# Performance work log

Hardware: AMD Instinct MI355X
Metric: run time of the kernel (lower is better)

Reference implementation:

```python
import jax, jax.numpy as jnp
import numpy as np
from jax import lax

EPS = 1e-5
BETA = 0.25  # commitment cost

def _conv(x, w, b):
    y = lax.conv_general_dilated(x, w, (1, 1), 'VALID',
                                 dimension_numbers=('NCHW', 'OIHW', 'NCHW'))
    return y + b[None, :, None, None]

def _maxpool2(x):
    return lax.reduce_window(x, -jnp.inf, lax.max, (1, 1, 2, 2), (1, 1, 2, 2), 'VALID')

def _bn(x, scale, bias):
    # training-mode batch norm over (N, H, W)
    mean = jnp.mean(x, axis=(0, 2, 3), keepdims=True)
    var = jnp.var(x, axis=(0, 2, 3), keepdims=True)
    xhat = (x - mean) * lax.rsqrt(var + EPS)
    return xhat * scale[None, :, None, None] + bias[None, :, None, None]

def _vq(z_nchw, codebook):
    # z: [B,32,4,4] -> vectors [B*16, 32]
    B, C, H, W = z_nchw.shape
    z = jnp.transpose(z_nchw, (0, 2, 3, 1)).reshape(-1, C)          # [N, D]
    # squared L2 distances to codebook [K, D]
    d = (jnp.sum(z * z, axis=1, keepdims=True)
         + jnp.sum(codebook * codebook, axis=1)
         - 2.0 * z @ codebook.T)                                    # [N, K]
    idx = jnp.argmin(d, axis=1)                                     # [N]
    q = codebook[idx]                                               # [N, D]
    sg = lax.stop_gradient
    vq_loss = jnp.mean((q - sg(z)) ** 2) + BETA * jnp.mean((sg(q) - z) ** 2)
    q_st = z + sg(q - z)                                            # straight-through
    recon = jnp.transpose(q_st.reshape(B, H, W, C), (0, 3, 1, 2))
    return recon, vq_loss

def setup_inputs() -> dict:
    key = jax.random.key(0)
    ks = jax.random.split(key, 12)
    f = lambda k, shape, s: (jax.random.normal(k, shape, jnp.float32) * s)
    inp = {
        'x': jax.random.normal(ks[0], (2048, 3, 32, 32), jnp.float32),
        'conv1_w': f(ks[1], (64, 3, 3, 3), 0.1), 'conv1_b': jnp.zeros((64,), jnp.float32),
        'bn1_scale': jnp.ones((64,), jnp.float32), 'bn1_bias': jnp.zeros((64,), jnp.float32),
        'conv2_w': f(ks[2], (32, 64, 3, 3), 0.05), 'conv2_b': jnp.zeros((32,), jnp.float32),
        'bn2_scale': jnp.ones((32,), jnp.float32), 'bn2_bias': jnp.zeros((32,), jnp.float32),
        'conv3_w': f(ks[3], (32, 32, 3, 3), 0.06), 'conv3_b': jnp.zeros((32,), jnp.float32),
        'bn3_scale': jnp.ones((32,), jnp.float32), 'bn3_bias': jnp.zeros((32,), jnp.float32),
        'codebook': f(ks[4], (100, 32), 0.5),
        'fc1_w': f(ks[5], (64, 512), 0.04), 'fc1_b': jnp.zeros((64,), jnp.float32),
        'fc2_w': f(ks[6], (10, 64), 0.12), 'fc2_b': jnp.zeros((10,), jnp.float32),
    }
    return inp

def reference(x, conv1_w, conv1_b, bn1_scale, bn1_bias,
              conv2_w, conv2_b, bn2_scale, bn2_bias,
              conv3_w, conv3_b, bn3_scale, bn3_bias,
              codebook, fc1_w, fc1_b, fc2_w, fc2_b):
    h = _bn(jax.nn.relu(_maxpool2(_conv(x, conv1_w, conv1_b))), bn1_scale, bn1_bias)
    h = _bn(jax.nn.relu(_maxpool2(_conv(h, conv2_w, conv2_b))), bn2_scale, bn2_bias)
    h = _bn(jax.nn.relu(_conv(h, conv3_w, conv3_b)), bn3_scale, bn3_bias)   # [B,32,4,4]
    recon, vq_loss = _vq(h, codebook)
    blended = 0.5 * recon + h
    flat = blended.reshape(-1, 4 * 4 * 32)
    z1 = jax.nn.relu(flat @ fc1_w.T + fc1_b)
    y = z1 @ fc2_w.T + fc2_b
    return recon, h, vq_loss, jax.nn.log_softmax(y, axis=1)
```

## Files before the change

kernel.cpp:

```cpp
#include <hip/hip_runtime.h>
#include <math.h>


#define CNT1 460800.0
#define CNT2 73728.0
#define CNT3 32768.0

__global__ void k0_w2t(const float* __restrict__ w2, float* __restrict__ w2t)
{
  const int idx = blockIdx.x * 256 + threadIdx.x;
  const int half = idx & 1, cog = (idx >> 1) & 15;
  const int r = (idx >> 5) % 72, cc = idx / 2304;
  const int o = cog + 16 * half;
  w2t[idx] = w2[o * 576 + cc * 72 + r];
}

template<int CB, int W4, int J0, int CNT>
__device__ __forceinline__ void conv1_seg(const float* img, const float* wr,
                                          int prow, float bias, float* vout)
{
  float acc[CNT][4];
#pragma unroll
  for (int j = 0; j < CNT; ++j) { acc[j][0] = 0; acc[j][1] = 0; acc[j][2] = 0; acc[j][3] = 0; }
#pragma unroll
  for (int cin = 0; cin < 3; ++cin) {
    float pt[4][4 * W4];
    const float4* src = (const float4*)&img[cin * 1024 + (2 * prow) * 32 + CB];
#pragma unroll
    for (int r = 0; r < 4; ++r)
#pragma unroll
      for (int u = 0; u < W4; ++u) {
        float4 f = src[r * 8 + u];
        pt[r][u * 4 + 0] = f.x; pt[r][u * 4 + 1] = f.y;
        pt[r][u * 4 + 2] = f.z; pt[r][u * 4 + 3] = f.w;
      }
#pragma unroll
    for (int jj = 0; jj < CNT; ++jj) {
      const int c0 = 2 * (J0 + jj) - CB;
#pragma unroll
      for (int kh = 0; kh < 3; ++kh)
#pragma unroll
        for (int kw = 0; kw < 3; ++kw) {
          const float w_ = wr[cin * 9 + kh * 3 + kw];
          acc[jj][0] += pt[kh][c0 + kw] * w_;
          acc[jj][1] += pt[kh][c0 + 1 + kw] * w_;
          acc[jj][2] += pt[kh + 1][c0 + kw] * w_;
          acc[jj][3] += pt[kh + 1][c0 + 1 + kw] * w_;
        }
    }
  }
#pragma unroll
  for (int jj = 0; jj < CNT; ++jj) {
    float v = fmaxf(fmaxf(acc[jj][0], acc[jj][1]), fmaxf(acc[jj][2], acc[jj][3])) + bias;
    vout[J0 + jj] = fmaxf(v, 0.f);
  }
}

__global__ __launch_bounds__(256) void k1_conv1(
    const float* __restrict__ x, const float* __restrict__ w1,
    const float* __restrict__ b1, double* __restrict__ dstats,
    float* __restrict__ y1)
{
  __shared__ float img[3072];
  __shared__ float red_s[256], red_q[256];
  const int n = blockIdx.x, t = threadIdx.x;
  const float4* xin = (const float4*)(x + n * 3072);
  float4* img4 = (float4*)img;
  for (int i = t; i < 768; i += 256) img4[i] = xin[i];
  const int ch = t & 63, rslot = t >> 6;
  float wr[27];
#pragma unroll
  for (int k = 0; k < 27; ++k) wr[k] = w1[ch * 27 + k];
  const float bias = b1[ch];
  __syncthreads();
  float s = 0.f, ss = 0.f;
  for (int prow = rslot; prow < 15; prow += 4) {
    float vout[15];
    conv1_seg<0, 4, 0, 7>(img, wr, prow, bias, vout);
    conv1_seg<12, 4, 7, 5>(img, wr, prow, bias, vout);
    conv1_seg<24, 2, 12, 3>(img, wr, prow, bias, vout);
    float4* dst = (float4*)(y1 + n * 15360 + ch * 240 + prow * 16);
    dst[0] = make_float4(vout[0], vout[1], vout[2], vout[3]);
    dst[1] = make_float4(vout[4], vout[5], vout[6], vout[7]);
    dst[2] = make_float4(vout[8], vout[9], vout[10], vout[11]);
    dst[3] = make_float4(vout[12], vout[13], vout[14], 0.f);
#pragma unroll
    for (int j = 0; j < 15; ++j) { s += vout[j]; ss += vout[j] * vout[j]; }
  }
  red_s[t] = s; red_q[t] = ss;
  __syncthreads();
  if (t < 64) {
    float rs = red_s[t] + red_s[t + 64] + red_s[t + 128] + red_s[t + 192];
    float rq = red_q[t] + red_q[t + 64] + red_q[t + 128] + red_q[t + 192];
    atomicAdd(&dstats[t * 16], (double)rs);
    atomicAdd(&dstats[t * 16 + 8], (double)rq);
  }
}

__global__ __launch_bounds__(256) void k1_conv1_stats(
    const float* __restrict__ x, const float* __restrict__ w1,
    const float* __restrict__ b1, double* __restrict__ dstats)
{
  __shared__ float img[3072];
  __shared__ float red[512];
  const int n = blockIdx.x, t = threadIdx.x;
  const float4* xin = (const float4*)(x + n * 3072);
  float4* img4 = (float4*)img;
  for (int i = t; i < 768; i += 256) img4[i] = xin[i];
  const int c = t >> 2, q = t & 3;
  float wr[27];
#pragma unroll
  for (int k = 0; k < 27; ++k) wr[k] = w1[c * 27 + k];
  const float bias = b1[c];
  __syncthreads();
  float s = 0.f, ss = 0.f;
  for (int p = q; p < 225; p += 4) {
    const int i = p / 15, j = p % 15;
    float a0 = 0, a1 = 0, a2 = 0, a3 = 0;
#pragma unroll
    for (int cin = 0; cin < 3; ++cin) {
      float pt[4][4];
#pragma unroll
      for (int r = 0; r < 4; ++r) {
        const float2* row = (const float2*)&img[cin * 1024 + (2 * i + r) * 32 + 2 * j];
        float2 u = row[0], v = row[1];
        pt[r][0] = u.x; pt[r][1] = u.y; pt[r][2] = v.x; pt[r][3] = v.y;
      }
#pragma unroll
      for (int kh = 0; kh < 3; ++kh)
#pragma unroll
        for (int kw = 0; kw < 3; ++kw) {
          const float wv = wr[cin * 9 + kh * 3 + kw];
          a0 += pt[kh][kw] * wv;     a1 += pt[kh][kw + 1] * wv;
          a2 += pt[kh + 1][kw] * wv; a3 += pt[kh + 1][kw + 1] * wv;
        }
    }
    float v = fmaxf(fmaxf(a0, a1), fmaxf(a2, a3)) + bias;
    v = fmaxf(v, 0.f);
    s += v; ss += v * v;
  }
  red[t * 2] = s; red[t * 2 + 1] = ss;
  __syncthreads();
  if (q == 0) {
    float rs = red[t * 2] + red[(t + 1) * 2] + red[(t + 2) * 2] + red[(t + 3) * 2];
    float rq = red[t * 2 + 1] + red[(t + 1) * 2 + 1] + red[(t + 2) * 2 + 1] + red[(t + 3) * 2 + 1];
    atomicAdd(&dstats[c * 16], (double)rs);
    atomicAdd(&dstats[c * 16 + 8], (double)rq);
  }
}

__global__ void k_finalize(const double* __restrict__ dstats,
                           const float* __restrict__ scale, const float* __restrict__ bias,
                           float* __restrict__ a, float* __restrict__ b, int C, double inv_cnt)
{
  int c = threadIdx.x;
  if (c < C) {
    double mean = dstats[c * 16] * inv_cnt;
    double var = dstats[c * 16 + 8] * inv_cnt - mean * mean;
    double ai = (double)scale[c] / sqrt(var + 1e-5);
    a[c] = (float)ai;
    b[c] = (float)((double)bias[c] - mean * ai);
  }
}

__global__ __launch_bounds__(384, 3) void k3_conv2_fast(
    const float* __restrict__ y1, const float* __restrict__ a1f,
    const float* __restrict__ b1f, const float* __restrict__ w2t,
    const float* __restrict__ b2, float* __restrict__ y2,
    double* __restrict__ dstats2)
{
  __shared__ float y1n[4 * 1928];
  __shared__ float w2c[72 * 32];
  __shared__ float sum2L[32], ss2L[32];
  const int t = threadIdx.x;
  const int n0 = blockIdx.x * 4;
  if (t < 32) { sum2L[t] = 0.f; ss2L[t] = 0.f; }
  const int irow = t / 64;
  const int img = (t >> 4) & 3;
  const int cog = t & 15;

  float acc[2][6][4];
#pragma unroll
  for (int h = 0; h < 2; ++h)
#pragma unroll
    for (int j = 0; j < 6; ++j) { acc[h][j][0] = 0; acc[h][j][1] = 0; acc[h][j][2] = 0; acc[h][j][3] = 0; }

  for (int cc = 0; cc < 8; ++cc) {
    __syncthreads();
    for (int idx = t; idx < 1920; idx += 384) {
      const int im = idx / 480, wi = idx - im * 480;
      const int ch = cc * 8 + wi / 60;
      const float an = a1f[ch], bn = b1f[ch];
      float4 v = ((const float4*)(y1 + (n0 + im) * 15360 + cc * 1920))[wi];
      v.x = an * v.x + bn; v.y = an * v.y + bn;
      v.z = an * v.z + bn; v.w = an * v.w + bn;
      ((float4*)y1n)[im * 482 + wi] = v;
    }
    for (int idx = t; idx < 576; idx += 384)
      ((float4*)w2c)[idx] = ((const float4*)(w2t + cc * 2304))[idx];
    __syncthreads();
    for (int ci = 0; ci < 8; ++ci) {
      float wv0[9], wv1[9];
#pragma unroll
      for (int s = 0; s < 9; ++s) {
        float2 wp = *(const float2*)&w2c[(ci * 9 + s) * 32 + cog * 2];
        wv0[s] = wp.x; wv1[s] = wp.y;
      }
      float pt[4][16];
      const float4* src = (const float4*)&y1n[img * 1928 + ci * 240 + 2 * irow * 16];
#pragma unroll
      for (int r = 0; r < 4; ++r)
#pragma unroll
        for (int u = 0; u < 4; ++u) {
          float4 f = src[r * 4 + u];
          pt[r][u * 4 + 0] = f.x; pt[r][u * 4 + 1] = f.y;
          pt[r][u * 4 + 2] = f.z; pt[r][u * 4 + 3] = f.w;
        }
#pragma unroll
      for (int j = 0; j < 6; ++j)
#pragma unroll
        for (int kh = 0; kh < 3; ++kh)
#pragma unroll
          for (int kw = 0; kw < 3; ++kw) {
            const float p00 = pt[kh][2 * j + kw],     p01 = pt[kh][2 * j + 1 + kw];
            const float p10 = pt[kh + 1][2 * j + kw], p11 = pt[kh + 1][2 * j + 1 + kw];
            const float w0 = wv0[kh * 3 + kw], w1_ = wv1[kh * 3 + kw];
            acc[0][j][0] += p00 * w0;  acc[0][j][1] += p01 * w0;
            acc[0][j][2] += p10 * w0;  acc[0][j][3] += p11 * w0;
            acc[1][j][0] += p00 * w1_; acc[1][j][1] += p01 * w1_;
            acc[1][j][2] += p10 * w1_; acc[1][j][3] += p11 * w1_;
          }
    }
  }
  const int n = n0 + img;
#pragma unroll
  for (int half = 0; half < 2; ++half) {
    const int co = cog + half * 16;
    const float bias = b2[co];
    float s = 0.f, sq = 0.f;
#pragma unroll
    for (int j = 0; j < 6; ++j) {
      float v = fmaxf(fmaxf(acc[half][j][0], acc[half][j][1]),
                      fmaxf(acc[half][j][2], acc[half][j][3])) + bias;
      v = fmaxf(v, 0.f);
      y2[n * 1152 + co * 36 + irow * 6 + j] = v;
      s += v; sq += v * v;
    }
    atomicAdd(&sum2L[co], s);
    atomicAdd(&ss2L[co], sq);
  }
  __syncthreads();
  if (t < 32) {
    atomicAdd(&dstats2[t * 16], (double)sum2L[t]);
    atomicAdd(&dstats2[t * 16 + 8], (double)ss2L[t]);
  }
}

__global__ __launch_bounds__(256) void k3_conv2(
    const float* __restrict__ x, const float* __restrict__ w1,
    const float* __restrict__ b1, const float* __restrict__ a1f,
    const float* __restrict__ b1f, const float* __restrict__ w2,
    const float* __restrict__ b2, float* __restrict__ y2,
    double* __restrict__ dstats2)
{
  __shared__ float img[3072];
  __shared__ float y1n[16 * 240];
  __shared__ float w2c[144 * 32];
  __shared__ float sum2L[32], ss2L[32];
  const int n = blockIdx.x, t = threadIdx.x;
  if (t < 32) { sum2L[t] = 0.f; ss2L[t] = 0.f; }
  const float4* xin = (const float4*)(x + n * 3072);
  float4* img4 = (float4*)img;
  for (int i = t; i < 768; i += 256) img4[i] = xin[i];

  const int co = t & 31, irow = t >> 5;
  const bool activeC = (irow < 6);

  float acc[6][4];
#pragma unroll
  for (int j = 0; j < 6; ++j) { acc[j][0] = 0; acc[j][1] = 0; acc[j][2] = 0; acc[j][3] = 0; }

  const int cA = t >> 4, qA = t & 15;

  for (int cc = 0; cc < 4; ++cc) {
    __syncthreads();
    {
      const int ch = cc * 16 + cA;
      float wr[27];
#pragma unroll
      for (int k = 0; k < 27; ++k) wr[k] = w1[ch * 27 + k];
      const float bias = b1[ch];
      const float an = a1f[ch], bn = b1f[ch];
      for (int p = qA; p < 225; p += 16) {
        const int i = p / 15, j = p % 15;
        float a0 = 0, a1 = 0, a2 = 0, a3 = 0;
#pragma unroll
        for (int cin = 0; cin < 3; ++cin) {
          float pt[4][4];
#pragma unroll
          for (int r = 0; r < 4; ++r) {
            const float2* row = (const float2*)&img[cin * 1024 + (2 * i + r) * 32 + 2 * j];
            float2 u = row[0], v = row[1];
            pt[r][0] = u.x; pt[r][1] = u.y; pt[r][2] = v.x; pt[r][3] = v.y;
          }
#pragma unroll
          for (int kh = 0; kh < 3; ++kh)
#pragma unroll
            for (int kw = 0; kw < 3; ++kw) {
              const float wv = wr[cin * 9 + kh * 3 + kw];
              a0 += pt[kh][kw] * wv;     a1 += pt[kh][kw + 1] * wv;
              a2 += pt[kh + 1][kw] * wv; a3 += pt[kh + 1][kw + 1] * wv;
            }
        }
        float v = fmaxf(fmaxf(a0, a1), fmaxf(a2, a3)) + bias;
        v = fmaxf(v, 0.f);
        y1n[cA * 240 + i * 16 + j] = an * v + bn;
      }
    }
    for (int idx = t; idx < 4608; idx += 256) {
      const int o = idx & 31, r = idx >> 5;
      w2c[r * 32 + o] = w2[o * 576 + cc * 144 + r];
    }
    __syncthreads();
    if (activeC) {
      for (int ci = 0; ci < 16; ++ci) {
        float wv[9];
#pragma unroll
        for (int s = 0; s < 9; ++s) wv[s] = w2c[(ci * 9 + s) * 32 + co];
        float pt[4][16];
        const float4* src = (const float4*)&y1n[ci * 240 + (2 * irow) * 16];
#pragma unroll
        for (int r = 0; r < 4; ++r)
#pragma unroll
          for (int u = 0; u < 4; ++u) {
            float4 f = src[r * 4 + u];
            pt[r][u * 4] = f.x; pt[r][u * 4 + 1] = f.y;
            pt[r][u * 4 + 2] = f.z; pt[r][u * 4 + 3] = f.w;
          }
#pragma unroll
        for (int j = 0; j < 6; ++j) {
#pragma unroll
          for (int kh = 0; kh < 3; ++kh)
#pragma unroll
            for (int kw = 0; kw < 3; ++kw) {
              const float w_ = wv[kh * 3 + kw];
              acc[j][0] += pt[kh][2 * j + kw] * w_;
              acc[j][1] += pt[kh][2 * j + 1 + kw] * w_;
              acc[j][2] += pt[kh + 1][2 * j + kw] * w_;
              acc[j][3] += pt[kh + 1][2 * j + 1 + kw] * w_;
            }
        }
      }
    }
  }
  if (activeC) {
    const float bias = b2[co];
    float s = 0.f, sq = 0.f;
#pragma unroll
    for (int j = 0; j < 6; ++j) {
      float v = fmaxf(fmaxf(acc[j][0], acc[j][1]), fmaxf(acc[j][2], acc[j][3])) + bias;
      v = fmaxf(v, 0.f);
      y2[n * 1152 + co * 36 + irow * 6 + j] = v;
      s += v; sq += v * v;
    }
    atomicAdd(&sum2L[co], s);
    atomicAdd(&ss2L[co], sq);
  }
  __syncthreads();
  if (t < 32) {
    atomicAdd(&dstats2[t * 16], (double)sum2L[t]);
    atomicAdd(&dstats2[t * 16 + 8], (double)ss2L[t]);
  }
}

__global__ __launch_bounds__(256) void k5_conv3(
    const float* __restrict__ y2, const float* __restrict__ a2f,
    const float* __restrict__ b2f, const float* __restrict__ w3,
    const float* __restrict__ b3, float* __restrict__ t3,
    double* __restrict__ dstats3)
{
  __shared__ float y2n[8 * 1152];
  __shared__ float w3c[144 * 32];
  __shared__ float sum3L[32], ss3L[32];
  const int blk = blockIdx.x, t = threadIdx.x;
  if (t < 32) { sum3L[t] = 0.f; ss3L[t] = 0.f; }
  for (int idx = t; idx < 9216; idx += 256) {
    const int ci = (idx % 1152) / 36;
    y2n[idx] = a2f[ci] * y2[blk * 9216 + idx] + b2f[ci];
  }
  const int il = t >> 5, c = t & 31;
  float acc[16];
#pragma unroll
  for (int p = 0; p < 16; ++p) acc[p] = 0.f;
  for (int ch = 0; ch < 2; ++ch) {
    __syncthreads();
    for (int idx = t; idx < 4608; idx += 256) {
      const int o = idx & 31, r = idx >> 5;
      w3c[r * 32 + o] = w3[o * 288 + ch * 144 + r];
    }
    __syncthreads();
    for (int ci = 0; ci < 16; ++ci) {
      float wv[9];
#pragma unroll
      for (int s = 0; s < 9; ++s) wv[s] = w3c[(ci * 9 + s) * 32 + c];
      float pt[36];
      const float4* src = (const float4*)&y2n[il * 1152 + (ch * 16 + ci) * 36];
#pragma unroll
      for (int u = 0; u < 9; ++u) {
        float4 f = src[u];
        pt[u * 4] = f.x; pt[u * 4 + 1] = f.y; pt[u * 4 + 2] = f.z; pt[u * 4 + 3] = f.w;
      }
#pragma unroll
      for (int i = 0; i < 4; ++i)
#pragma unroll
        for (int j = 0; j < 4; ++j) {
          float a_ = 0.f;
#pragma unroll
          for (int kh = 0; kh < 3; ++kh)
#pragma unroll
            for (int kw = 0; kw < 3; ++kw)
              a_ += pt[(i + kh) * 6 + j + kw] * wv[kh * 3 + kw];
          acc[i * 4 + j] += a_;
        }
    }
  }
  const float bias = b3[c];
  float s = 0.f, sq = 0.f;
  float vout[16];
#pragma unroll
  for (int p = 0; p < 16; ++p) {
    float v = fmaxf(acc[p] + bias, 0.f);
    vout[p] = v; s += v; sq += v * v;
  }
  const int n = blk * 8 + il;
  float4* dst = (float4*)&t3[(n * 32 + c) * 16];
#pragma unroll
  for (int u = 0; u < 4; ++u)
    dst[u] = make_float4(vout[u * 4], vout[u * 4 + 1], vout[u * 4 + 2], vout[u * 4 + 3]);
  atomicAdd(&sum3L[c], s);
  atomicAdd(&ss3L[c], sq);
  __syncthreads();
  if (t < 32) {
    atomicAdd(&dstats3[t * 16], (double)sum3L[t]);
    atomicAdd(&dstats3[t * 16 + 8], (double)ss3L[t]);
  }
}

__global__ __launch_bounds__(256) void k8_vq(
    const float* __restrict__ t3, const float* __restrict__ a3f,
    const float* __restrict__ b3f, const float* __restrict__ cbg,
    float* __restrict__ recon, float* __restrict__ hout,
    double* __restrict__ dloss)
{
  __shared__ float cb[3200];
  __shared__ float n2[100];
  const int t = threadIdx.x;
  for (int i = t; i < 3200; i += 256) cb[i] = cbg[i];
  __syncthreads();
  if (t < 100) {
    float s = 0.f;
#pragma unroll
    for (int c = 0; c < 32; ++c) { float v = cb[t * 32 + c]; s += v * v; }
    n2[t] = s;
  }
  __syncthreads();
  const int v = blockIdx.x * 256 + t;
  const int b = v >> 4, p = v & 15;
  float z[32];
  float z2 = 0.f;
#pragma unroll
  for (int c = 0; c < 32; ++c) {
    const float zz = a3f[c] * t3[b * 512 + c * 16 + p] + b3f[c];
    hout[b * 512 + c * 16 + p] = zz;
    z[c] = zz; z2 += zz * zz;
  }
  float best = 1e30f; int bi = 0;
  for (int k = 0; k < 100; ++k) {
    float dot = 0.f;
#pragma unroll
    for (int c = 0; c < 32; ++c) dot += z[c] * cb[k * 32 + c];
    const float d = z2 + n2[k] - 2.f * dot;
    if (d < best) { best = d; bi = k; }
  }
  float lsum = 0.f;
#pragma unroll
  for (int c = 0; c < 32; ++c) {
    const float qv = cb[bi * 32 + c];
    recon[b * 512 + c * 16 + p] = qv;
    const float df = qv - z[c];
    lsum += df * df;
  }
#pragma unroll
  for (int off = 32; off > 0; off >>= 1) lsum += __shfl_down(lsum, off, 64);
  if ((t & 63) == 0) atomicAdd(dloss, (double)lsum);
}

__global__ __launch_bounds__(256) void k10_fc(
    const float* __restrict__ recon, const float* __restrict__ h,
    const float* __restrict__ fc1w, const float* __restrict__ fc1b,
    const float* __restrict__ fc2w, const float* __restrict__ fc2b,
    float* __restrict__ out, const double* __restrict__ dloss,
    float* __restrict__ loss_out)
{
  __shared__ float flat[4 * 512];
  __shared__ float z1[4 * 64];
  __shared__ float yL[4 * 10];
  const int t = threadIdx.x;
  const int w = t >> 6, l = t & 63;
  const int n = blockIdx.x * 4 + w;
  if (blockIdx.x == 0 && t == 0)
    loss_out[0] = (float)(1.25 * dloss[0] / (32768.0 * 32.0));
  for (int k = l; k < 512; k += 64)
    flat[w * 512 + k] = 0.5f * recon[n * 512 + k] + h[n * 512 + k];
  __syncthreads();
  float acc = fc1b[l];
  const float4* wrow = (const float4*)(fc1w + l * 512);
  const float4* frow = (const float4*)(flat + w * 512);
  for (int k4 = 0; k4 < 128; ++k4) {
    const float4 wv = wrow[k4], fv = frow[k4];
    acc += wv.x * fv.x + wv.y * fv.y + wv.z * fv.z + wv.w * fv.w;
  }
  z1[w * 64 + l] = fmaxf(acc, 0.f);
  __syncthreads();
  if (l < 10) {
    float a = fc2b[l];
#pragma unroll
    for (int i = 0; i < 64; ++i) a += fc2w[l * 64 + i] * z1[w * 64 + i];
    yL[w * 10 + l] = a;
  }
  __syncthreads();
  if (l < 10) {
    float m = -1e30f;
#pragma unroll
    for (int i = 0; i < 10; ++i) m = fmaxf(m, yL[w * 10 + i]);
    float s = 0.f;
#pragma unroll
    for (int i = 0; i < 10; ++i) s += expf(yL[w * 10 + i] - m);
    out[n * 10 + l] = yL[w * 10 + l] - m - logf(s);
  }
}

extern "C" void kernel_launch(void* const* d_in, const int* in_sizes, int n_in,
                              void* d_out, int out_size, void* d_ws, size_t ws_size,
                              hipStream_t stream)
{
  (void)in_sizes; (void)n_in; (void)out_size;
  const float* x    = (const float*)d_in[0];
  const float* w1   = (const float*)d_in[1];
  const float* cb1  = (const float*)d_in[2];
  const float* bn1s = (const float*)d_in[3];
  const float* bn1b = (const float*)d_in[4];
  const float* w2   = (const float*)d_in[5];
  const float* cb2  = (const float*)d_in[6];
  const float* bn2s = (const float*)d_in[7];
  const float* bn2b = (const float*)d_in[8];
  const float* w3   = (const float*)d_in[9];
  const float* cb3  = (const float*)d_in[10];
  const float* bn3s = (const float*)d_in[11];
  const float* bn3b = (const float*)d_in[12];
  const float* cbk  = (const float*)d_in[13];
  const float* fc1w = (const float*)d_in[14];
  const float* fc1b = (const float*)d_in[15];
  const float* fc2w = (const float*)d_in[16];
  const float* fc2b = (const float*)d_in[17];
  float* out = (float*)d_out;

  double* dstats = (double*)d_ws;
  float* fws = (float*)((char*)d_ws + 32768);
  float* a1 = fws;        float* b1 = fws + 64;
  float* a2 = fws + 128;  float* b2 = fws + 160;
  float* a3 = fws + 192;  float* b3 = fws + 224;

  float* recon_out = out;
  float* h_out     = out + 1048576;
  float* loss_out  = out + 2097152;
  float* y_out     = out + 2097153;

  const bool fast = ws_size >= 139568128ull;

  hipMemsetAsync(d_ws, 0, 32768, stream);

  if (fast) {
    float* w2t = fws + 256;
    float* y2  = fws + 256 + 18432;
    float* t3  = y2 + 2359296;
    float* y1  = t3 + 1048576;

    k0_w2t<<<72, 256, 0, stream>>>(w2, w2t);
    k1_conv1<<<2048, 256, 0, stream>>>(x, w1, cb1, dstats, y1);
    k_finalize<<<1, 64, 0, stream>>>(dstats, bn1s, bn1b, a1, b1, 64, 1.0 / CNT1);
    k3_conv2_fast<<<512, 384, 0, stream>>>(y1, a1, b1, w2t, cb2, y2, dstats + 1024);
    k_finalize<<<1, 64, 0, stream>>>(dstats + 1024, bn2s, bn2b, a2, b2, 32, 1.0 / CNT2);
    k5_conv3<<<256, 256, 0, stream>>>(y2, a2, b2, w3, cb3, t3, dstats + 1536);
    k_finalize<<<1, 64, 0, stream>>>(dstats + 1536, bn3s, bn3b, a3, b3, 32, 1.0 / CNT3);
    k8_vq<<<128, 256, 0, stream>>>(t3, a3, b3, cbk, recon_out, h_out, dstats + 2048);
    k10_fc<<<512, 256, 0, stream>>>(recon_out, h_out, fc1w, fc1b, fc2w, fc2b,
                                    y_out, dstats + 2048, loss_out);
  } else {
    float* y2 = fws + 256;
    float* t3 = fws + 256 + 2359296;

    k1_conv1_stats<<<2048, 256, 0, stream>>>(x, w1, cb1, dstats);
    k_finalize<<<1, 64, 0, stream>>>(dstats, bn1s, bn1b, a1, b1, 64, 1.0 / CNT1);
    k3_conv2<<<2048, 256, 0, stream>>>(x, w1, cb1, a1, b1, w2, cb2, y2, dstats + 1024);
    k_finalize<<<1, 64, 0, stream>>>(dstats + 1024, bn2s, bn2b, a2, b2, 32, 1.0 / CNT2);
    k5_conv3<<<256, 256, 0, stream>>>(y2, a2, b2, w3, cb3, t3, dstats + 1536);
    k_finalize<<<1, 64, 0, stream>>>(dstats + 1536, bn3s, bn3b, a3, b3, 32, 1.0 / CNT3);
    k8_vq<<<128, 256, 0, stream>>>(t3, a3, b3, cbk, recon_out, h_out, dstats + 2048);
    k10_fc<<<512, 256, 0, stream>>>(recon_out, h_out, fc1w, fc1b, fc2w, fc2b,
                                    y_out, dstats + 2048, loss_out);
  }
}
```

Measured before the change: 462.4 us.

## Fold BN1 into conv2 weights, fuse BN finalizes, prefetch conv2 tiles

Conv1 now has each thread compute two output channels at once, so the input patch registers are shared, and it writes outputs per segment. BN1 is folded algebraically into the conv2 weights and an effective bias by a prep kernel. This removes the per-element normalization in conv2 and two separate finalize/transpose launches. The BN2 and BN3 finalize steps are computed inside the conv3 and VQ kernels, cutting several tiny launches. Conv2 also prefetches the next chunk of y1 and weights into registers while computing, and its occupancy hint is dropped, which may raise register pressure.

```diff
diff --git a/kernel.cpp b/kernel.cpp
--- a/kernel.cpp
+++ b/kernel.cpp
@@ -6,22 +6,17 @@
 #define CNT2 73728.0
 #define CNT3 32768.0
 
-__global__ void k0_w2t(const float* __restrict__ w2, float* __restrict__ w2t)
-{
-  const int idx = blockIdx.x * 256 + threadIdx.x;
-  const int half = idx & 1, cog = (idx >> 1) & 15;
-  const int r = (idx >> 5) % 72, cc = idx / 2304;
-  const int o = cog + 16 * half;
-  w2t[idx] = w2[o * 576 + cc * 72 + r];
-}
-
-template<int CB, int W4, int J0, int CNT>
-__device__ __forceinline__ void conv1_seg(const float* img, const float* wr,
-                                          int prow, float bias, float* vout)
-{
-  float acc[CNT][4];
-#pragma unroll
-  for (int j = 0; j < CNT; ++j) { acc[j][0] = 0; acc[j][1] = 0; acc[j][2] = 0; acc[j][3] = 0; }
+template<int CB, int W4, int J0, int CNTJ>
+__device__ __forceinline__ void conv1_seg2(
+    const float* img, const float* wr0, const float* wr1, int prow,
+    float bias0, float bias1, float* row0, float* row1,
+    float& s0, float& ss0, float& s1, float& ss1)
+{
+  float acc[2][CNTJ][4];
+#pragma unroll
+  for (int h = 0; h < 2; ++h)
+#pragma unroll
+    for (int j = 0; j < CNTJ; ++j) { acc[h][j][0] = 0; acc[h][j][1] = 0; acc[h][j][2] = 0; acc[h][j][3] = 0; }
 #pragma unroll
   for (int cin = 0; cin < 3; ++cin) {
     float pt[4][4 * W4];
@@ -35,25 +30,35 @@
         pt[r][u * 4 + 2] = f.z; pt[r][u * 4 + 3] = f.w;
       }
 #pragma unroll
-    for (int jj = 0; jj < CNT; ++jj) {
+    for (int jj = 0; jj < CNTJ; ++jj) {
       const int c0 = 2 * (J0 + jj) - CB;
 #pragma unroll
       for (int kh = 0; kh < 3; ++kh)
 #pragma unroll
         for (int kw = 0; kw < 3; ++kw) {
-          const float w_ = wr[cin * 9 + kh * 3 + kw];
-          acc[jj][0] += pt[kh][c0 + kw] * w_;
-          acc[jj][1] += pt[kh][c0 + 1 + kw] * w_;
-          acc[jj][2] += pt[kh + 1][c0 + kw] * w_;
-          acc[jj][3] += pt[kh + 1][c0 + 1 + kw] * w_;
+          const float p00 = pt[kh][c0 + kw],     p01 = pt[kh][c0 + 1 + kw];
+          const float p10 = pt[kh + 1][c0 + kw], p11 = pt[kh + 1][c0 + 1 + kw];
+          const float w0 = wr0[cin * 9 + kh * 3 + kw];
+          const float w1_ = wr1[cin * 9 + kh * 3 + kw];
+          acc[0][jj][0] += p00 * w0;  acc[0][jj][1] += p01 * w0;
+          acc[0][jj][2] += p10 * w0;  acc[0][jj][3] += p11 * w0;
+          acc[1][jj][0] += p00 * w1_; acc[1][jj][1] += p01 * w1_;
+          acc[1][jj][2] += p10 * w1_; acc[1][jj][3] += p11 * w1_;
         }
     }
   }
-#pragma unroll
-  for (int jj = 0; jj < CNT; ++jj) {
-    float v = fmaxf(fmaxf(acc[jj][0], acc[jj][1]), fmaxf(acc[jj][2], acc[jj][3])) + bias;
-    vout[J0 + jj] = fmaxf(v, 0.f);
-  }
+  float v0[4] = {0, 0, 0, 0}, v1[4] = {0, 0, 0, 0};
+#pragma unroll
+  for (int jj = 0; jj < CNTJ; ++jj) {
+    float a = fmaxf(fmaxf(acc[0][jj][0], acc[0][jj][1]), fmaxf(acc[0][jj][2], acc[0][jj][3])) + bias0;
+    a = fmaxf(a, 0.f);
+    v0[jj] = a; s0 += a; ss0 += a * a;
+    float b = fmaxf(fmaxf(acc[1][jj][0], acc[1][jj][1]), fmaxf(acc[1][jj][2], acc[1][jj][3])) + bias1;
+    b = fmaxf(b, 0.f);
+    v1[jj] = b; s1 += b; ss1 += b * b;
+  }
+  *(float4*)(row0 + J0) = make_float4(v0[0], v0[1], v0[2], v0[3]);
+  *(float4*)(row1 + J0) = make_float4(v1[0], v1[1], v1[2], v1[3]);
 }
 
 __global__ __launch_bounds__(256) void k1_conv1(
@@ -62,36 +67,34 @@
     float* __restrict__ y1)
 {
   __shared__ float img[3072];
-  __shared__ float red_s[256], red_q[256];
   const int n = blockIdx.x, t = threadIdx.x;
   const float4* xin = (const float4*)(x + n * 3072);
   float4* img4 = (float4*)img;
   for (int i = t; i < 768; i += 256) img4[i] = xin[i];
-  const int ch = t & 63, rslot = t >> 6;
-  float wr[27];
-#pragma unroll
-  for (int k = 0; k < 27; ++k) wr[k] = w1[ch * 27 + k];
-  const float bias = b1[ch];
-  __syncthreads();
-  float s = 0.f, ss = 0.f;
-  for (int prow = rslot; prow < 15; prow += 4) {
-    float vout[15];
-    conv1_seg<0, 4, 0, 7>(img, wr, prow, bias, vout);
-    conv1_seg<12, 4, 7, 5>(img, wr, prow, bias, vout);
-    conv1_seg<24, 2, 12, 3>(img, wr, prow, bias, vout);
-    float4* dst = (float4*)(y1 + n * 15360 + ch * 240 + prow * 16);
-    dst[0] = make_float4(vout[0], vout[1], vout[2], vout[3]);
-    dst[1] = make_float4(vout[4], vout[5], vout[6], vout[7]);
-    dst[2] = make_float4(vout[8], vout[9], vout[10], vout[11]);
-    dst[3] = make_float4(vout[12], vout[13], vout[14], 0.f);
-#pragma unroll
-    for (int j = 0; j < 15; ++j) { s += vout[j]; ss += vout[j] * vout[j]; }
-  }
-  red_s[t] = s; red_q[t] = ss;
+  const int cog = t & 31, rslot = t >> 5;
+  float wr0[27], wr1[27];
+#pragma unroll
+  for (int k = 0; k < 27; ++k) { wr0[k] = w1[cog * 27 + k]; wr1[k] = w1[(cog + 32) * 27 + k]; }
+  const float bias0 = b1[cog], bias1 = b1[cog + 32];
+  __syncthreads();
+  float s0 = 0.f, ss0 = 0.f, s1 = 0.f, ss1 = 0.f;
+  for (int prow = rslot; prow < 15; prow += 8) {
+    float* row0 = y1 + n * 15360 + cog * 240 + prow * 16;
+    float* row1 = y1 + n * 15360 + (cog + 32) * 240 + prow * 16;
+    conv1_seg2<0, 3, 0, 4>(img, wr0, wr1, prow, bias0, bias1, row0, row1, s0, ss0, s1, ss1);
+    conv1_seg2<8, 3, 4, 4>(img, wr0, wr1, prow, bias0, bias1, row0, row1, s0, ss0, s1, ss1);
+    conv1_seg2<16, 3, 8, 4>(img, wr0, wr1, prow, bias0, bias1, row0, row1, s0, ss0, s1, ss1);
+    conv1_seg2<24, 2, 12, 3>(img, wr0, wr1, prow, bias0, bias1, row0, row1, s0, ss0, s1, ss1);
+  }
+  __syncthreads();
+  float* red = img;
+  red[t] = s0; red[256 + t] = ss0; red[512 + t] = s1; red[768 + t] = ss1;
   __syncthreads();
   if (t < 64) {
-    float rs = red_s[t] + red_s[t + 64] + red_s[t + 128] + red_s[t + 192];
-    float rq = red_q[t] + red_q[t + 64] + red_q[t + 128] + red_q[t + 192];
+    const int base = (t < 32) ? t : (512 + (t - 32));
+    float rs = 0.f, rq = 0.f;
+#pragma unroll
+    for (int k = 0; k < 8; ++k) { rs += red[base + 32 * k]; rq += red[base + 256 + 32 * k]; }
     atomicAdd(&dstats[t * 16], (double)rs);
     atomicAdd(&dstats[t * 16 + 8], (double)rq);
   }
@@ -163,10 +166,42 @@
   }
 }
 
-__global__ __launch_bounds__(384, 3) void k3_conv2_fast(
-    const float* __restrict__ y1, const float* __restrict__ a1f,
-    const float* __restrict__ b1f, const float* __restrict__ w2t,
-    const float* __restrict__ b2, float* __restrict__ y2,
+__global__ void k2b_prep(const float* __restrict__ w2, const float* __restrict__ b2,
+                         const float* __restrict__ bn1s, const float* __restrict__ bn1b,
+                         const double* __restrict__ dstats,
+                         float* __restrict__ w2s, float* __restrict__ b2eff)
+{
+  const int idx = blockIdx.x * 256 + threadIdx.x;
+  const int half = idx & 1, cog = (idx >> 1) & 15;
+  const int r = (idx >> 5) % 72, cc = idx / 2304;
+  const int o = cog + 16 * half;
+  const int ci = cc * 8 + r / 9, s = r % 9;
+  {
+    double mean = dstats[ci * 16] / CNT1;
+    double var = dstats[ci * 16 + 8] / CNT1 - mean * mean;
+    float ai = (float)((double)bn1s[ci] / sqrt(var + 1e-5));
+    w2s[idx] = w2[o * 576 + ci * 9 + s] * ai;
+  }
+  if (blockIdx.x == 0 && threadIdx.x < 32) {
+    const int co = threadIdx.x;
+    float c = b2[co];
+    for (int cj = 0; cj < 64; ++cj) {
+      double mean = dstats[cj * 16] / CNT1;
+      double var = dstats[cj * 16 + 8] / CNT1 - mean * mean;
+      double ai = (double)bn1s[cj] / sqrt(var + 1e-5);
+      float bf = (float)((double)bn1b[cj] - mean * ai);
+      float wsum = 0.f;
+#pragma unroll
+      for (int s2 = 0; s2 < 9; ++s2) wsum += w2[co * 576 + cj * 9 + s2];
+      c += bf * wsum;
+    }
+    b2eff[co] = c;
+  }
+}
+
+__global__ __launch_bounds__(384) void k3_conv2_fast(
+    const float* __restrict__ y1, const float* __restrict__ w2s,
+    const float* __restrict__ b2eff, float* __restrict__ y2,
     double* __restrict__ dstats2)
 {
   __shared__ float y1n[4 * 1928];
@@ -185,20 +220,43 @@
 #pragma unroll
     for (int j = 0; j < 6; ++j) { acc[h][j][0] = 0; acc[h][j][1] = 0; acc[h][j][2] = 0; acc[h][j][3] = 0; }
 
+  float4 ry[5], rw[2];
+#pragma unroll
+  for (int k = 0; k < 5; ++k) {
+    const int idx = t + 384 * k, im = idx / 480, wi = idx - im * 480;
+    ry[k] = ((const float4*)(y1 + (n0 + im) * 15360))[wi];
+  }
+#pragma unroll
+  for (int k = 0; k < 2; ++k) {
+    const int idx = t + 384 * k;
+    if (idx < 576) rw[k] = ((const float4*)w2s)[idx];
+  }
+
   for (int cc = 0; cc < 8; ++cc) {
     __syncthreads();
-    for (int idx = t; idx < 1920; idx += 384) {
-      const int im = idx / 480, wi = idx - im * 480;
-      const int ch = cc * 8 + wi / 60;
-      const float an = a1f[ch], bn = b1f[ch];
-      float4 v = ((const float4*)(y1 + (n0 + im) * 15360 + cc * 1920))[wi];
-      v.x = an * v.x + bn; v.y = an * v.y + bn;
-      v.z = an * v.z + bn; v.w = an * v.w + bn;
-      ((float4*)y1n)[im * 482 + wi] = v;
-    }
-    for (int idx = t; idx < 576; idx += 384)
-      ((float4*)w2c)[idx] = ((const float4*)(w2t + cc * 2304))[idx];
+#pragma unroll
+    for (int k = 0; k < 5; ++k) {
+      const int idx = t + 384 * k, im = idx / 480, wi = idx - im * 480;
+      ((float4*)y1n)[im * 482 + wi] = ry[k];
+    }
+#pragma unroll
+    for (int k = 0; k < 2; ++k) {
+      const int idx = t + 384 * k;
+      if (idx < 576) ((float4*)w2c)[idx] = rw[k];
+    }
     __syncthreads();
+    if (cc < 7) {
+#pragma unroll
+      for (int k = 0; k < 5; ++k) {
+        const int idx = t + 384 * k, im = idx / 480, wi = idx - im * 480;
+        ry[k] = ((const float4*)(y1 + (n0 + im) * 15360 + (cc + 1) * 1920))[wi];
+      }
+#pragma unroll
+      for (int k = 0; k < 2; ++k) {
+        const int idx = t + 384 * k;
+        if (idx < 576) rw[k] = ((const float4*)(w2s + (cc + 1) * 2304))[idx];
+      }
+    }
     for (int ci = 0; ci < 8; ++ci) {
       float wv0[9], wv1[9];
 #pragma unroll
@@ -236,7 +294,7 @@
 #pragma unroll
   for (int half = 0; half < 2; ++half) {
     const int co = cog + half * 16;
-    const float bias = b2[co];
+    const float bias = b2eff[co];
     float s = 0.f, sq = 0.f;
 #pragma unroll
     for (int j = 0; j < 6; ++j) {
@@ -374,19 +432,28 @@
 }
 
 __global__ __launch_bounds__(256) void k5_conv3(
-    const float* __restrict__ y2, const float* __restrict__ a2f,
-    const float* __restrict__ b2f, const float* __restrict__ w3,
-    const float* __restrict__ b3, float* __restrict__ t3,
-    double* __restrict__ dstats3)
+    const float* __restrict__ y2, const double* __restrict__ dstats2,
+    const float* __restrict__ bn2s, const float* __restrict__ bn2b,
+    const float* __restrict__ w3, const float* __restrict__ b3,
+    float* __restrict__ t3, double* __restrict__ dstats3)
 {
   __shared__ float y2n[8 * 1152];
   __shared__ float w3c[144 * 32];
+  __shared__ float a2s[32], b2s[32];
   __shared__ float sum3L[32], ss3L[32];
   const int blk = blockIdx.x, t = threadIdx.x;
-  if (t < 32) { sum3L[t] = 0.f; ss3L[t] = 0.f; }
+  if (t < 32) {
+    sum3L[t] = 0.f; ss3L[t] = 0.f;
+    double mean = dstats2[t * 16] / CNT2;
+    double var = dstats2[t * 16 + 8] / CNT2 - mean * mean;
+    double ai = (double)bn2s[t] / sqrt(var + 1e-5);
+    a2s[t] = (float)ai;
+    b2s[t] = (float)((double)bn2b[t] - mean * ai);
+  }
+  __syncthreads();
   for (int idx = t; idx < 9216; idx += 256) {
     const int ci = (idx % 1152) / 36;
-    y2n[idx] = a2f[ci] * y2[blk * 9216 + idx] + b2f[ci];
+    y2n[idx] = a2s[ci] * y2[blk * 9216 + idx] + b2s[ci];
   }
   const int il = t >> 5, c = t & 31;
   float acc[16];
@@ -447,15 +514,23 @@
 }
 
 __global__ __launch_bounds__(256) void k8_vq(
-    const float* __restrict__ t3, const float* __restrict__ a3f,
-    const float* __restrict__ b3f, const float* __restrict__ cbg,
-    float* __restrict__ recon, float* __restrict__ hout,
-    double* __restrict__ dloss)
+    const float* __restrict__ t3, const double* __restrict__ dstats3,
+    const float* __restrict__ bn3s, const float* __restrict__ bn3b,
+    const float* __restrict__ cbg, float* __restrict__ recon,
+    float* __restrict__ hout, double* __restrict__ dloss)
 {
   __shared__ float cb[3200];
   __shared__ float n2[100];
+  __shared__ float a3s[32], b3s[32];
   const int t = threadIdx.x;
   for (int i = t; i < 3200; i += 256) cb[i] = cbg[i];
+  if (t < 32) {
+    double mean = dstats3[t * 16] / CNT3;
+    double var = dstats3[t * 16 + 8] / CNT3 - mean * mean;
+    double ai = (double)bn3s[t] / sqrt(var + 1e-5);
+    a3s[t] = (float)ai;
+    b3s[t] = (float)((double)bn3b[t] - mean * ai);
+  }
   __syncthreads();
   if (t < 100) {
     float s = 0.f;
@@ -470,7 +545,7 @@
   float z2 = 0.f;
 #pragma unroll
   for (int c = 0; c < 32; ++c) {
-    const float zz = a3f[c] * t3[b * 512 + c * 16 + p] + b3f[c];
+    const float zz = a3s[c] * t3[b * 512 + c * 16 + p] + b3s[c];
     hout[b * 512 + c * 16 + p] = zz;
     z[c] = zz; z2 += zz * zz;
   }
@@ -568,8 +643,7 @@
   double* dstats = (double*)d_ws;
   float* fws = (float*)((char*)d_ws + 32768);
   float* a1 = fws;        float* b1 = fws + 64;
-  float* a2 = fws + 128;  float* b2 = fws + 160;
-  float* a3 = fws + 192;  float* b3 = fws + 224;
+  float* b2eff = fws + 128;
 
   float* recon_out = out;
   float* h_out     = out + 1048576;
@@ -581,19 +655,16 @@
   hipMemsetAsync(d_ws, 0, 32768, stream);
 
   if (fast) {
-    float* w2t = fws + 256;
+    float* w2s = fws + 256;
     float* y2  = fws + 256 + 18432;
     float* t3  = y2 + 2359296;
     float* y1  = t3 + 1048576;
 
-    k0_w2t<<<72, 256, 0, stream>>>(w2, w2t);
     k1_conv1<<<2048, 256, 0, stream>>>(x, w1, cb1, dstats, y1);
-    k_finalize<<<1, 64, 0, stream>>>(dstats, bn1s, bn1b, a1, b1, 64, 1.0 / CNT1);
-    k3_conv2_fast<<<512, 384, 0, stream>>>(y1, a1, b1, w2t, cb2, y2, dstats + 1024);
-    k_finalize<<<1, 64, 0, stream>>>(dstats + 1024, bn2s, bn2b, a2, b2, 32, 1.0 / CNT2);
-    k5_conv3<<<256, 256, 0, stream>>>(y2, a2, b2, w3, cb3, t3, dstats + 1536);
-    k_finalize<<<1, 64, 0, stream>>>(dstats + 1536, bn3s, bn3b, a3, b3, 32, 1.0 / CNT3);
-    k8_vq<<<128, 256, 0, stream>>>(t3, a3, b3, cbk, recon_out, h_out, dstats + 2048);
+    k2b_prep<<<72, 256, 0, stream>>>(w2, cb2, bn1s, bn1b, dstats, w2s, b2eff);
+    k3_conv2_fast<<<512, 384, 0, stream>>>(y1, w2s, b2eff, y2, dstats + 1024);
+    k5_conv3<<<256, 256, 0, stream>>>(y2, dstats + 1024, bn2s, bn2b, w3, cb3, t3, dstats + 1536);
+    k8_vq<<<128, 256, 0, stream>>>(t3, dstats + 1536, bn3s, bn3b, cbk, recon_out, h_out, dstats + 2048);
     k10_fc<<<512, 256, 0, stream>>>(recon_out, h_out, fc1w, fc1b, fc2w, fc2b,
                                     y_out, dstats + 2048, loss_out);
   } else {
@@ -603,10 +674,8 @@
     k1_conv1_stats<<<2048, 256, 0, stream>>>(x, w1, cb1, dstats);
     k_finalize<<<1, 64, 0, stream>>>(dstats, bn1s, bn1b, a1, b1, 64, 1.0 / CNT1);
     k3_conv2<<<2048, 256, 0, stream>>>(x, w1, cb1, a1, b1, w2, cb2, y2, dstats + 1024);
-    k_finalize<<<1, 64, 0, stream>>>(dstats + 1024, bn2s, bn2b, a2, b2, 32, 1.0 / CNT2);
-    k5_conv3<<<256, 256, 0, stream>>>(y2, a2, b2, w3, cb3, t3, dstats + 1536);
-    k_finalize<<<1, 64, 0, stream>>>(dstats + 1536, bn3s, bn3b, a3, b3, 32, 1.0 / CNT3);
-    k8_vq<<<128, 256, 0, stream>>>(t3, a3, b3, cbk, recon_out, h_out, dstats + 2048);
+    k5_conv3<<<256, 256, 0, stream>>>(y2, dstats + 1024, bn2s, bn2b, w3, cb3, t3, dstats + 1536);
+    k8_vq<<<128, 256, 0, stream>>>(t3, dstats + 1536, bn3s, bn3b, cbk, recon_out, h_out, dstats + 2048);
     k10_fc<<<512, 256, 0, stream>>>(recon_out, h_out, fc1w, fc1b, fc2w, fc2b,
                                     y_out, dstats + 2048, loss_out);
   }
```

After: 548.5 us. 1.19x slower.

## Fold BN1 affine into conv2 weights and inline BN finalize into consumers

Applied to the files above, without the earlier changes.

Removes the separate k_finalize launches. BN2 and BN3 scale and shift are now computed per block inside conv3 and VQ. BN1 is folded algebraically into the transposed conv2 weights and an effective bias by a prep kernel that replaces the old weight-transpose kernel, so conv2 no longer applies the affine per element while staging. This saves several tiny launches and the per-element FMA in conv2 staging. In exchange it adds redundant per-block stat computation and a serial 64-iteration bias loop, changes float rounding order, and drops the occupancy hint from conv2's launch bounds.

```diff
diff --git a/kernel.cpp b/kernel.cpp
--- a/kernel.cpp
+++ b/kernel.cpp
@@ -5,15 +5,6 @@
 #define CNT1 460800.0
 #define CNT2 73728.0
 #define CNT3 32768.0
-
-__global__ void k0_w2t(const float* __restrict__ w2, float* __restrict__ w2t)
-{
-  const int idx = blockIdx.x * 256 + threadIdx.x;
-  const int half = idx & 1, cog = (idx >> 1) & 15;
-  const int r = (idx >> 5) % 72, cc = idx / 2304;
-  const int o = cog + 16 * half;
-  w2t[idx] = w2[o * 576 + cc * 72 + r];
-}
 
 template<int CB, int W4, int J0, int CNT>
 __device__ __forceinline__ void conv1_seg(const float* img, const float* wr,
@@ -163,10 +154,42 @@
   }
 }
 
-__global__ __launch_bounds__(384, 3) void k3_conv2_fast(
-    const float* __restrict__ y1, const float* __restrict__ a1f,
-    const float* __restrict__ b1f, const float* __restrict__ w2t,
-    const float* __restrict__ b2, float* __restrict__ y2,
+__global__ void k2b_prep(const float* __restrict__ w2, const float* __restrict__ b2,
+                         const float* __restrict__ bn1s, const float* __restrict__ bn1b,
+                         const double* __restrict__ dstats,
+                         float* __restrict__ w2s, float* __restrict__ b2eff)
+{
+  const int idx = blockIdx.x * 256 + threadIdx.x;
+  const int half = idx & 1, cog = (idx >> 1) & 15;
+  const int r = (idx >> 5) % 72, cc = idx / 2304;
+  const int o = cog + 16 * half;
+  const int ci = cc * 8 + r / 9, s = r % 9;
+  {
+    double mean = dstats[ci * 16] / CNT1;
+    double var = dstats[ci * 16 + 8] / CNT1 - mean * mean;
+    float ai = (float)((double)bn1s[ci] / sqrt(var + 1e-5));
+    w2s[idx] = w2[o * 576 + ci * 9 + s] * ai;
+  }
+  if (blockIdx.x == 0 && threadIdx.x < 32) {
+    const int co = threadIdx.x;
+    float c = b2[co];
+    for (int cj = 0; cj < 64; ++cj) {
+      double mean = dstats[cj * 16] / CNT1;
+      double var = dstats[cj * 16 + 8] / CNT1 - mean * mean;
+      double ai = (double)bn1s[cj] / sqrt(var + 1e-5);
+      float bf = (float)((double)bn1b[cj] - mean * ai);
+      float wsum = 0.f;
+#pragma unroll
+      for (int s2 = 0; s2 < 9; ++s2) wsum += w2[co * 576 + cj * 9 + s2];
+      c += bf * wsum;
+    }
+    b2eff[co] = c;
+  }
+}
+
+__global__ __launch_bounds__(384) void k3_conv2_fast(
+    const float* __restrict__ y1, const float* __restrict__ w2s,
+    const float* __restrict__ b2eff, float* __restrict__ y2,
     double* __restrict__ dstats2)
 {
   __shared__ float y1n[4 * 1928];
@@ -189,15 +212,11 @@
     __syncthreads();
     for (int idx = t; idx < 1920; idx += 384) {
       const int im = idx / 480, wi = idx - im * 480;
-      const int ch = cc * 8 + wi / 60;
-      const float an = a1f[ch], bn = b1f[ch];
-      float4 v = ((const float4*)(y1 + (n0 + im) * 15360 + cc * 1920))[wi];
-      v.x = an * v.x + bn; v.y = an * v.y + bn;
-      v.z = an * v.z + bn; v.w = an * v.w + bn;
-      ((float4*)y1n)[im * 482 + wi] = v;
+      ((float4*)y1n)[im * 482 + wi] =
+          ((const float4*)(y1 + (n0 + im) * 15360 + cc * 1920))[wi];
     }
     for (int idx = t; idx < 576; idx += 384)
-      ((float4*)w2c)[idx] = ((const float4*)(w2t + cc * 2304))[idx];
+      ((float4*)w2c)[idx] = ((const float4*)(w2s + cc * 2304))[idx];
     __syncthreads();
     for (int ci = 0; ci < 8; ++ci) {
       float wv0[9], wv1[9];
@@ -236,7 +255,7 @@
 #pragma unroll
   for (int half = 0; half < 2; ++half) {
     const int co = cog + half * 16;
-    const float bias = b2[co];
+    const float bias = b2eff[co];
     float s = 0.f, sq = 0.f;
 #pragma unroll
     for (int j = 0; j < 6; ++j) {
@@ -374,19 +393,28 @@
 }
 
 __global__ __launch_bounds__(256) void k5_conv3(
-    const float* __restrict__ y2, const float* __restrict__ a2f,
-    const float* __restrict__ b2f, const float* __restrict__ w3,
-    const float* __restrict__ b3, float* __restrict__ t3,
-    double* __restrict__ dstats3)
+    const float* __restrict__ y2, const double* __restrict__ dstats2,
+    const float* __restrict__ bn2s, const float* __restrict__ bn2b,
+    const float* __restrict__ w3, const float* __restrict__ b3,
+    float* __restrict__ t3, double* __restrict__ dstats3)
 {
   __shared__ float y2n[8 * 1152];
   __shared__ float w3c[144 * 32];
+  __shared__ float a2s[32], b2s[32];
   __shared__ float sum3L[32], ss3L[32];
   const int blk = blockIdx.x, t = threadIdx.x;
-  if (t < 32) { sum3L[t] = 0.f; ss3L[t] = 0.f; }
+  if (t < 32) {
+    sum3L[t] = 0.f; ss3L[t] = 0.f;
+    double mean = dstats2[t * 16] / CNT2;
+    double var = dstats2[t * 16 + 8] / CNT2 - mean * mean;
+    double ai = (double)bn2s[t] / sqrt(var + 1e-5);
+    a2s[t] = (float)ai;
+    b2s[t] = (float)((double)bn2b[t] - mean * ai);
+  }
+  __syncthreads();
   for (int idx = t; idx < 9216; idx += 256) {
     const int ci = (idx % 1152) / 36;
-    y2n[idx] = a2f[ci] * y2[blk * 9216 + idx] + b2f[ci];
+    y2n[idx] = a2s[ci] * y2[blk * 9216 + idx] + b2s[ci];
   }
   const int il = t >> 5, c = t & 31;
   float acc[16];
@@ -447,15 +475,23 @@
 }
 
 __global__ __launch_bounds__(256) void k8_vq(
-    const float* __restrict__ t3, const float* __restrict__ a3f,
-    const float* __restrict__ b3f, const float* __restrict__ cbg,
-    float* __restrict__ recon, float* __restrict__ hout,
-    double* __restrict__ dloss)
+    const float* __restrict__ t3, const double* __restrict__ dstats3,
+    const float* __restrict__ bn3s, const float* __restrict__ bn3b,
+    const float* __restrict__ cbg, float* __restrict__ recon,
+    float* __restrict__ hout, double* __restrict__ dloss)
 {
   __shared__ float cb[3200];
   __shared__ float n2[100];
+  __shared__ float a3s[32], b3s[32];
   const int t = threadIdx.x;
   for (int i = t; i < 3200; i += 256) cb[i] = cbg[i];
+  if (t < 32) {
+    double mean = dstats3[t * 16] / CNT3;
+    double var = dstats3[t * 16 + 8] / CNT3 - mean * mean;
+    double ai = (double)bn3s[t] / sqrt(var + 1e-5);
+    a3s[t] = (float)ai;
+    b3s[t] = (float)((double)bn3b[t] - mean * ai);
+  }
   __syncthreads();
   if (t < 100) {
     float s = 0.f;
@@ -470,7 +506,7 @@
   float z2 = 0.f;
 #pragma unroll
   for (int c = 0; c < 32; ++c) {
-    const float zz = a3f[c] * t3[b * 512 + c * 16 + p] + b3f[c];
+    const float zz = a3s[c] * t3[b * 512 + c * 16 + p] + b3s[c];
     hout[b * 512 + c * 16 + p] = zz;
     z[c] = zz; z2 += zz * zz;
   }
@@ -568,8 +604,7 @@
   double* dstats = (double*)d_ws;
   float* fws = (float*)((char*)d_ws + 32768);
   float* a1 = fws;        float* b1 = fws + 64;
-  float* a2 = fws + 128;  float* b2 = fws + 160;
-  float* a3 = fws + 192;  float* b3 = fws + 224;
+  float* b2eff = fws + 128;
 
   float* recon_out = out;
   float* h_out     = out + 1048576;
@@ -581,19 +616,16 @@
   hipMemsetAsync(d_ws, 0, 32768, stream);
 
   if (fast) {
-    float* w2t = fws + 256;
+    float* w2s = fws + 256;
     float* y2  = fws + 256 + 18432;
     float* t3  = y2 + 2359296;
     float* y1  = t3 + 1048576;
 
-    k0_w2t<<<72, 256, 0, stream>>>(w2, w2t);
     k1_conv1<<<2048, 256, 0, stream>>>(x, w1, cb1, dstats, y1);
-    k_finalize<<<1, 64, 0, stream>>>(dstats, bn1s, bn1b, a1, b1, 64, 1.0 / CNT1);
-    k3_conv2_fast<<<512, 384, 0, stream>>>(y1, a1, b1, w2t, cb2, y2, dstats + 1024);
-    k_finalize<<<1, 64, 0, stream>>>(dstats + 1024, bn2s, bn2b, a2, b2, 32, 1.0 / CNT2);
-    k5_conv3<<<256, 256, 0, stream>>>(y2, a2, b2, w3, cb3, t3, dstats + 1536);
-    k_finalize<<<1, 64, 0, stream>>>(dstats + 1536, bn3s, bn3b, a3, b3, 32, 1.0 / CNT3);
-    k8_vq<<<128, 256, 0, stream>>>(t3, a3, b3, cbk, recon_out, h_out, dstats + 2048);
+    k2b_prep<<<72, 256, 0, stream>>>(w2, cb2, bn1s, bn1b, dstats, w2s, b2eff);
+    k3_conv2_fast<<<512, 384, 0, stream>>>(y1, w2s, b2eff, y2, dstats + 1024);
+    k5_conv3<<<256, 256, 0, stream>>>(y2, dstats + 1024, bn2s, bn2b, w3, cb3, t3, dstats + 1536);
+    k8_vq<<<128, 256, 0, stream>>>(t3, dstats + 1536, bn3s, bn3b, cbk, recon_out, h_out, dstats + 2048);
     k10_fc<<<512, 256, 0, stream>>>(recon_out, h_out, fc1w, fc1b, fc2w, fc2b,
                                     y_out, dstats + 2048, loss_out);
   } else {
@@ -603,10 +635,8 @@
     k1_conv1_stats<<<2048, 256, 0, stream>>>(x, w1, cb1, dstats);
     k_finalize<<<1, 64, 0, stream>>>(dstats, bn1s, bn1b, a1, b1, 64, 1.0 / CNT1);
     k3_conv2<<<2048, 256, 0, stream>>>(x, w1, cb1, a1, b1, w2, cb2, y2, dstats + 1024);
-    k_finalize<<<1, 64, 0, stream>>>(dstats + 1024, bn2s, bn2b, a2, b2, 32, 1.0 / CNT2);
-    k5_conv3<<<256, 256, 0, stream>>>(y2, a2, b2, w3, cb3, t3, dstats + 1536);
-    k_finalize<<<1, 64, 0, stream>>>(dstats + 1536, bn3s, bn3b, a3, b3, 32, 1.0 / CNT3);
-    k8_vq<<<128, 256, 0, stream>>>(t3, a3, b3, cbk, recon_out, h_out, dstats + 2048);
+    k5_conv3<<<256, 256, 0, stream>>>(y2, dstats + 1024, bn2s, bn2b, w3, cb3, t3, dstats + 1536);
+    k8_vq<<<128, 256, 0, stream>>>(t3, dstats + 1536, bn3s, bn3b, cbk, recon_out, h_out, dstats + 2048);
     k10_fc<<<512, 256, 0, stream>>>(recon_out, h_out, fc1w, fc1b, fc2w, fc2b,
                                     y_out, dstats + 2048, loss_out);
   }
```

Result: slower. 481.5 us (+4.1%).
